# Performance work log

Hardware: AMD Instinct MI355X
Metric: run time of the kernel (lower is better)

The kernel has to match this reference:

```python
import jax, jax.numpy as jnp
import numpy as np

NODE_DIM = 64
OUT_DIM = 64
EDGE_DIM = 64
N_NODES = 50000
N_EDGES = 800000
BN_EPS = 1e-5


def _batchnorm(x, gamma, beta):
    # training-mode BatchNorm1d: biased batch statistics
    mean = jnp.mean(x, axis=0)
    var = jnp.mean((x - mean) ** 2, axis=0)
    return (x - mean) * jax.lax.rsqrt(var + BN_EPS) * gamma + beta


def setup_inputs() -> dict:
    key = jax.random.key(0)
    ks = jax.random.split(key, 16)
    s = 0.05  # weight init scale
    inp = {
        "em": jax.random.normal(ks[0], (N_NODES, NODE_DIM), jnp.float32),
        "edge_index": jax.random.randint(ks[1], (2, N_EDGES), 0, N_NODES, jnp.int64),
        "edge_features": jax.random.normal(ks[2], (N_EDGES, EDGE_DIM), jnp.float32),
        # GINEConv edge linear (edge_dim -> node_dim)
        "W_le": jax.random.normal(ks[3], (EDGE_DIM, NODE_DIM), jnp.float32) * s,
        "b_le": jnp.zeros((NODE_DIM,), jnp.float32),
        # GINEConv nn: Linear(node_dim, out) -> ReLU -> Linear(out, out)
        "W1": jax.random.normal(ks[4], (NODE_DIM, OUT_DIM), jnp.float32) * s,
        "b1": jnp.zeros((OUT_DIM,), jnp.float32),
        "W2": jax.random.normal(ks[5], (OUT_DIM, OUT_DIM), jnp.float32) * s,
        "b2": jnp.zeros((OUT_DIM,), jnp.float32),
        # x BatchNorm affine
        "gx": jnp.ones((OUT_DIM,), jnp.float32),
        "bx": jnp.zeros((OUT_DIM,), jnp.float32),
        # edge MLP: (edge_dim + 2*out) -> out -> out -> out
        "We1": jax.random.normal(ks[6], (EDGE_DIM + 2 * OUT_DIM, OUT_DIM), jnp.float32) * s,
        "be1": jnp.zeros((OUT_DIM,), jnp.float32),
        "We2": jax.random.normal(ks[7], (OUT_DIM, OUT_DIM), jnp.float32) * s,
        "be2": jnp.zeros((OUT_DIM,), jnp.float32),
        "We3": jax.random.normal(ks[8], (OUT_DIM, OUT_DIM), jnp.float32) * s,
        "be3": jnp.zeros((OUT_DIM,), jnp.float32),
        # edge BatchNorm affine
        "ge": jnp.ones((OUT_DIM,), jnp.float32),
        "be": jnp.zeros((OUT_DIM,), jnp.float32),
    }
    return inp


def reference(em, edge_index, edge_features, W_le, b_le, W1, b1, W2, b2, gx, bx,
              We1, be1, We2, be2, We3, be3, ge, be):
    src, dst = edge_index[0], edge_index[1]
    # GINEConv: msg = relu(x_j + lin(edge_attr)), sum-aggregated at target
    msg = jax.nn.relu(em[src] + edge_features @ W_le + b_le)  # [E, node_dim]
    aggr = jax.ops.segment_sum(msg, dst, num_segments=em.shape[0])  # [N, node_dim]
    h = em + aggr  # eps = 0
    h = jax.nn.relu(h @ W1 + b1) @ W2 + b2  # [N, out]
    x_em = jax.nn.relu(_batchnorm(h, gx, bx))
    # edge update: concat(x_em[src], x_em[dst], edge_features)
    edge_mess = jnp.concatenate([x_em[src], x_em[dst], edge_features], axis=1)
    e = jax.nn.relu(edge_mess @ We1 + be1)
    e = jax.nn.relu(e @ We2 + be2)
    e = e @ We3 + be3
    edge_out = jax.nn.relu(_batchnorm(e, ge, be))
    return x_em, edge_out
```

## Files before the change

### kernel.cpp

```cpp
#include <hip/hip_runtime.h>
#include <cstddef>

#define NN 50000
#define NE 800000

typedef __bf16 bf16x8 __attribute__((ext_vector_type(8)));
typedef float  f32x4  __attribute__((ext_vector_type(4)));

__device__ __forceinline__ bf16x8 ldfrag(const __bf16* __restrict__ wfr, int f, int lane) {
    return *reinterpret_cast<const bf16x8*>(wfr + (size_t)(f * 64 + lane) * 8);
}
__device__ __forceinline__ f32x4 mfma16(bf16x8 a, bf16x8 b, f32x4 c) {
    return __builtin_amdgcn_mfma_f32_16x16x32_bf16(a, b, c, 0, 0, 0);
}
__device__ __forceinline__ bool idx_is64(const int* eidx) {
    return ((eidx[1] | eidx[3] | eidx[5] | eidx[7]) == 0);
}
__device__ __forceinline__ int ld_src(const int* eidx, bool is64, int e) {
    return is64 ? eidx[(size_t)2 * e] : eidx[e];
}
__device__ __forceinline__ int ld_dst(const int* eidx, bool is64, int e) {
    return is64 ? eidx[2 * ((size_t)NE + e)] : eidx[(size_t)NE + e];
}

__global__ __launch_bounds__(256) void prep(const float* __restrict__ wle, const float* __restrict__ w1,
                                            const float* __restrict__ w2, const float* __restrict__ we1,
                                            const float* __restrict__ we2, const float* __restrict__ we3,
                                            __bf16* __restrict__ wfr) {
    int sid = blockIdx.x * 256 + threadIdx.x;
    int f = sid >> 6, lane = sid & 63;
    const float* W; int fo;
    if (f < 8)       { W = wle; fo = 0; }
    else if (f < 16) { W = w1;  fo = 8; }
    else if (f < 24) { W = w2;  fo = 16; }
    else if (f < 48) { W = we1; fo = 24; }
    else if (f < 56) { W = we2; fo = 48; }
    else             { W = we3; fo = 56; }
    int lf = f - fo, kt = lf >> 2, nt = lf & 3;
    int g = lane >> 4, c = lane & 15;
#pragma unroll
    for (int b = 0; b < 8; b++) {
        int k = kt * 32 + g * 8 + b;
        int n = nt * 16 + c;
        wfr[(size_t)(f * 64 + lane) * 8 + b] = (__bf16)W[(size_t)k * 64 + n];
    }
}

__global__ __launch_bounds__(256) void k1(const float* __restrict__ em, const int* __restrict__ eidx,
                                          const float* __restrict__ ef, const __bf16* __restrict__ wfr,
                                          const float* __restrict__ ble, float* __restrict__ nodebuf) {
    __shared__ __bf16 Ash[64][72];
    const int t = threadIdx.x;
    const int base = blockIdx.x * 64;
    {
        const int r = t >> 2, seg = t & 3;
        const float4* p = reinterpret_cast<const float4*>(ef + (size_t)(base + r) * 64 + seg * 16);
#pragma unroll
        for (int i = 0; i < 4; i++) {
            float4 v = p[i];
            int cb = seg * 16 + i * 4;
            Ash[r][cb + 0] = (__bf16)v.x; Ash[r][cb + 1] = (__bf16)v.y;
            Ash[r][cb + 2] = (__bf16)v.z; Ash[r][cb + 3] = (__bf16)v.w;
        }
    }
    const bool is64 = idx_is64(eidx);
    __syncthreads();
    const int lane = t & 63, w = t >> 6, c = lane & 15, g = lane >> 4;
    const int arow = w * 16 + c;
    f32x4 acc[4] = {{0.f,0.f,0.f,0.f},{0.f,0.f,0.f,0.f},{0.f,0.f,0.f,0.f},{0.f,0.f,0.f,0.f}};
#pragma unroll
    for (int kt = 0; kt < 2; kt++) {
        bf16x8 a = *reinterpret_cast<const bf16x8*>(&Ash[arow][kt * 32 + g * 8]);
#pragma unroll
        for (int nt = 0; nt < 4; nt++) acc[nt] = mfma16(a, ldfrag(wfr, kt * 4 + nt, lane), acc[nt]);
    }
#pragma unroll
    for (int rr = 0; rr < 4; rr++) {
        int e = base + w * 16 + g * 4 + rr;
        int sn = ld_src(eidx, is64, e);
        int dn = ld_dst(eidx, is64, e);
#pragma unroll
        for (int nt = 0; nt < 4; nt++) {
            int col = nt * 16 + c;
            float v = acc[nt][rr] + ble[col] + em[(size_t)sn * 64 + col];
            if (v > 0.f) atomicAdd(&nodebuf[(size_t)dn * 64 + col], v);
        }
    }
}

__global__ __launch_bounds__(256) void k2(const float* __restrict__ em, float* __restrict__ nb,
                                          const __bf16* __restrict__ wfr, const float* __restrict__ b1,
                                          const float* __restrict__ b2, float* __restrict__ sums) {
    __shared__ __bf16 Ash[64][72];
    __shared__ __bf16 Ysh[64][72];
    __shared__ float bs[128];
    const int t = threadIdx.x;
    const int base = blockIdx.x * 64;
    if (t < 128) bs[t] = 0.f;
    {
        const int r = t >> 2, seg = t & 3;
        const int row = base + r;
        if (row < NN) {
            const float4* pe = reinterpret_cast<const float4*>(em + (size_t)row * 64 + seg * 16);
            const float4* pa = reinterpret_cast<const float4*>(nb + (size_t)row * 64 + seg * 16);
#pragma unroll
            for (int i = 0; i < 4; i++) {
                float4 a = pe[i], b = pa[i];
                int cb = seg * 16 + i * 4;
                Ash[r][cb + 0] = (__bf16)(a.x + b.x); Ash[r][cb + 1] = (__bf16)(a.y + b.y);
                Ash[r][cb + 2] = (__bf16)(a.z + b.z); Ash[r][cb + 3] = (__bf16)(a.w + b.w);
            }
        } else {
#pragma unroll
            for (int j = 0; j < 16; j++) Ash[r][seg * 16 + j] = (__bf16)0.f;
        }
    }
    __syncthreads();
    const int lane = t & 63, w = t >> 6, c = lane & 15, g = lane >> 4;
    const int arow = w * 16 + c;
    f32x4 a1[4] = {{0.f,0.f,0.f,0.f},{0.f,0.f,0.f,0.f},{0.f,0.f,0.f,0.f},{0.f,0.f,0.f,0.f}};
#pragma unroll
    for (int kt = 0; kt < 2; kt++) {
        bf16x8 a = *reinterpret_cast<const bf16x8*>(&Ash[arow][kt * 32 + g * 8]);
#pragma unroll
        for (int nt = 0; nt < 4; nt++) a1[nt] = mfma16(a, ldfrag(wfr, 8 + kt * 4 + nt, lane), a1[nt]);
    }
#pragma unroll
    for (int nt = 0; nt < 4; nt++) {
        float bb = b1[nt * 16 + c];
#pragma unroll
        for (int rr = 0; rr < 4; rr++) {
            float v = a1[nt][rr] + bb;
            v = v > 0.f ? v : 0.f;
            Ysh[w * 16 + g * 4 + rr][nt * 16 + c] = (__bf16)v;
        }
    }
    __syncthreads();
    f32x4 a2[4] = {{0.f,0.f,0.f,0.f},{0.f,0.f,0.f,0.f},{0.f,0.f,0.f,0.f},{0.f,0.f,0.f,0.f}};
#pragma unroll
    for (int kt = 0; kt < 2; kt++) {
        bf16x8 a = *reinterpret_cast<const bf16x8*>(&Ysh[arow][kt * 32 + g * 8]);
#pragma unroll
        for (int nt = 0; nt < 4; nt++) a2[nt] = mfma16(a, ldfrag(wfr, 16 + kt * 4 + nt, lane), a2[nt]);
    }
#pragma unroll
    for (int nt = 0; nt < 4; nt++) {
        int col = nt * 16 + c;
        float bb = b2[col];
        float ss = 0.f, qq = 0.f;
#pragma unroll
        for (int rr = 0; rr < 4; rr++) {
            int row = base + w * 16 + g * 4 + rr;
            if (row < NN) {
                float v = a2[nt][rr] + bb;
                nb[(size_t)row * 64 + col] = v;
                ss += v; qq += v * v;
            }
        }
        ss += __shfl_xor(ss, 16); ss += __shfl_xor(ss, 32);
        qq += __shfl_xor(qq, 16); qq += __shfl_xor(qq, 32);
        if (g == 0) { atomicAdd(&bs[col], ss); atomicAdd(&bs[64 + col], qq); }
    }
    __syncthreads();
    if (t < 128) atomicAdd(&sums[t], bs[t]);
}

__global__ __launch_bounds__(256) void k3(float* __restrict__ nb, const float* __restrict__ sums,
                                          const float* __restrict__ gx, const float* __restrict__ bx,
                                          __bf16* __restrict__ wsx) {
    size_t i4 = (size_t)(blockIdx.x * 256 + threadIdx.x) * 4;
    int col0 = (int)(i4 & 63);
    float4 v = *reinterpret_cast<const float4*>(nb + i4);
    const float* pv = reinterpret_cast<const float*>(&v);
    float o[4]; short so[4];
#pragma unroll
    for (int j = 0; j < 4; j++) {
        int col = col0 + j;
        float m   = sums[col] * (1.0f / 50000.0f);
        float var = sums[64 + col] * (1.0f / 50000.0f) - m * m;
        float inv = rsqrtf(var + 1e-5f);
        float x = (pv[j] - m) * inv * gx[col] + bx[col];
        x = x > 0.f ? x : 0.f;
        o[j] = x;
        so[j] = __builtin_bit_cast(short, (__bf16)x);
    }
    *reinterpret_cast<float4*>(nb + i4) = make_float4(o[0], o[1], o[2], o[3]);
    *reinterpret_cast<short4*>(wsx + i4) = make_short4(so[0], so[1], so[2], so[3]);
}

__global__ __launch_bounds__(256) void k4(const int* __restrict__ eidx, const float* __restrict__ ef,
                                          const __bf16* __restrict__ wsx, const __bf16* __restrict__ wfr,
                                          const float* __restrict__ be1, const float* __restrict__ be2,
                                          const float* __restrict__ be3, float* __restrict__ eout,
                                          float* __restrict__ pws) {
    __shared__ __bf16 Ash[64][200];
    __shared__ __bf16 Ysh[64][72];
    __shared__ float bs[128];
    const int t = threadIdx.x;
    const int base = blockIdx.x * 64;
    if (t < 128) bs[t] = 0.f;
    const bool is64 = idx_is64(eidx);
    {
        const int r = t >> 2, seg = t & 3;
        const int e = base + r;
        const int sn = ld_src(eidx, is64, e);
        const int dn = ld_dst(eidx, is64, e);
        const uint4* ps = reinterpret_cast<const uint4*>(wsx + ((size_t)sn << 6)) + seg * 2;
        const uint4* pd = reinterpret_cast<const uint4*>(wsx + ((size_t)dn << 6)) + seg * 2;
        *reinterpret_cast<uint4*>(&Ash[r][seg * 16]) = ps[0];
        *reinterpret_cast<uint4*>(&Ash[r][seg * 16 + 8]) = ps[1];
        *reinterpret_cast<uint4*>(&Ash[r][64 + seg * 16]) = pd[0];
        *reinterpret_cast<uint4*>(&Ash[r][64 + seg * 16 + 8]) = pd[1];
        const float4* pf = reinterpret_cast<const float4*>(ef + (size_t)e * 64 + seg * 16);
#pragma unroll
        for (int i = 0; i < 4; i++) {
            float4 v = pf[i];
            int cb = 128 + seg * 16 + i * 4;
            Ash[r][cb + 0] = (__bf16)v.x; Ash[r][cb + 1] = (__bf16)v.y;
            Ash[r][cb + 2] = (__bf16)v.z; Ash[r][cb + 3] = (__bf16)v.w;
        }
    }
    __syncthreads();
    const int lane = t & 63, w = t >> 6, c = lane & 15, g = lane >> 4;
    const int arow = w * 16 + c;
    f32x4 a1[4] = {{0.f,0.f,0.f,0.f},{0.f,0.f,0.f,0.f},{0.f,0.f,0.f,0.f},{0.f,0.f,0.f,0.f}};
#pragma unroll
    for (int kt = 0; kt < 6; kt++) {
        bf16x8 a = *reinterpret_cast<const bf16x8*>(&Ash[arow][kt * 32 + g * 8]);
#pragma unroll
        for (int nt = 0; nt < 4; nt++) a1[nt] = mfma16(a, ldfrag(wfr, 24 + kt * 4 + nt, lane), a1[nt]);
    }
#pragma unroll
    for (int nt = 0; nt < 4; nt++) {
        float bb = be1[nt * 16 + c];
#pragma unroll
        for (int rr = 0; rr < 4; rr++) {
            float v = a1[nt][rr] + bb;
            v = v > 0.f ? v : 0.f;
            Ysh[w * 16 + g * 4 + rr][nt * 16 + c] = (__bf16)v;
        }
    }
    __syncthreads();
    f32x4 a2[4] = {{0.f,0.f,0.f,0.f},{0.f,0.f,0.f,0.f},{0.f,0.f,0.f,0.f},{0.f,0.f,0.f,0.f}};
#pragma unroll
    for (int kt = 0; kt < 2; kt++) {
        bf16x8 a = *reinterpret_cast<const bf16x8*>(&Ysh[arow][kt * 32 + g * 8]);
#pragma unroll
        for (int nt = 0; nt < 4; nt++) a2[nt] = mfma16(a, ldfrag(wfr, 48 + kt * 4 + nt, lane), a2[nt]);
    }
    __syncthreads();
#pragma unroll
    for (int nt = 0; nt < 4; nt++) {
        float bb = be2[nt * 16 + c];
#pragma unroll
        for (int rr = 0; rr < 4; rr++) {
            float v = a2[nt][rr] + bb;
            v = v > 0.f ? v : 0.f;
            Ysh[w * 16 + g * 4 + rr][nt * 16 + c] = (__bf16)v;
        }
    }
    __syncthreads();
    f32x4 a3[4] = {{0.f,0.f,0.f,0.f},{0.f,0.f,0.f,0.f},{0.f,0.f,0.f,0.f},{0.f,0.f,0.f,0.f}};
#pragma unroll
    for (int kt = 0; kt < 2; kt++) {
        bf16x8 a = *reinterpret_cast<const bf16x8*>(&Ysh[arow][kt * 32 + g * 8]);
#pragma unroll
        for (int nt = 0; nt < 4; nt++) a3[nt] = mfma16(a, ldfrag(wfr, 56 + kt * 4 + nt, lane), a3[nt]);
    }
#pragma unroll
    for (int nt = 0; nt < 4; nt++) {
        int col = nt * 16 + c;
        float bb = be3[col];
        float ss = 0.f, qq = 0.f;
#pragma unroll
        for (int rr = 0; rr < 4; rr++) {
            int e = base + w * 16 + g * 4 + rr;
            float v = a3[nt][rr] + bb;
            eout[(size_t)e * 64 + col] = v;
            ss += v; qq += v * v;
        }
        ss += __shfl_xor(ss, 16); ss += __shfl_xor(ss, 32);
        qq += __shfl_xor(qq, 16); qq += __shfl_xor(qq, 32);
        if (g == 0) { atomicAdd(&bs[col], ss); atomicAdd(&bs[64 + col], qq); }
    }
    __syncthreads();
    if (t < 128) pws[(size_t)t * 12500 + blockIdx.x] = bs[t];
}

__global__ __launch_bounds__(256) void k4r(const float* __restrict__ pws, float* __restrict__ sums) {
    int b = blockIdx.x;
    float s = 0.f;
    for (int i = threadIdx.x; i < 12500; i += 256) s += pws[(size_t)b * 12500 + i];
#pragma unroll
    for (int m = 32; m >= 1; m >>= 1) s += __shfl_xor(s, m);
    __shared__ float acc4[4];
    int lane = threadIdx.x & 63, wid = threadIdx.x >> 6;
    if (lane == 0) acc4[wid] = s;
    __syncthreads();
    if (threadIdx.x == 0) sums[128 + b] = acc4[0] + acc4[1] + acc4[2] + acc4[3];
}

__global__ __launch_bounds__(256) void k5(float* __restrict__ eo, const float* __restrict__ sums,
                                          const float* __restrict__ ge, const float* __restrict__ be) {
    size_t i4 = (size_t)(blockIdx.x * 256 + threadIdx.x) * 4;
    int col0 = (int)(i4 & 63);
    float4 v = *reinterpret_cast<const float4*>(eo + i4);
    const float* pv = reinterpret_cast<const float*>(&v);
    float o[4];
#pragma unroll
    for (int j = 0; j < 4; j++) {
        int col = col0 + j;
        float m   = sums[128 + col] * (1.0f / 800000.0f);
        float var = sums[192 + col] * (1.0f / 800000.0f) - m * m;
        float inv = rsqrtf(var + 1e-5f);
        float x = (pv[j] - m) * inv * ge[col] + be[col];
        o[j] = x > 0.f ? x : 0.f;
    }
    *reinterpret_cast<float4*>(eo + i4) = make_float4(o[0], o[1], o[2], o[3]);
}

extern "C" void kernel_launch(void* const* d_in, const int* in_sizes, int n_in,
                              void* d_out, int out_size, void* d_ws, size_t ws_size,
                              hipStream_t stream) {
    const float* em   = (const float*)d_in[0];
    const int*   eidx = (const int*)d_in[1];
    const float* ef   = (const float*)d_in[2];
    const float* W_le = (const float*)d_in[3];
    const float* b_le = (const float*)d_in[4];
    const float* W1   = (const float*)d_in[5];
    const float* b1   = (const float*)d_in[6];
    const float* W2   = (const float*)d_in[7];
    const float* b2   = (const float*)d_in[8];
    const float* gx   = (const float*)d_in[9];
    const float* bx   = (const float*)d_in[10];
    const float* We1  = (const float*)d_in[11];
    const float* be1  = (const float*)d_in[12];
    const float* We2  = (const float*)d_in[13];
    const float* be2  = (const float*)d_in[14];
    const float* We3  = (const float*)d_in[15];
    const float* be3  = (const float*)d_in[16];
    const float* ge   = (const float*)d_in[17];
    const float* be   = (const float*)d_in[18];

    float* out = (float*)d_out;
    float* nodebuf = out;
    float* eout = out + (size_t)NN * 64;

    float*  sums = (float*)d_ws;
    __bf16* wfr  = (__bf16*)((char*)d_ws + 1024);
    __bf16* wsx  = (__bf16*)((char*)d_ws + 1024 + 65536);
    float*  pws  = (float*)((char*)d_ws + 1024 + 65536 + (size_t)NN * 64 * 2);

    hipMemsetAsync(sums, 0, 256 * sizeof(float), stream);
    hipMemsetAsync(nodebuf, 0, (size_t)NN * 64 * sizeof(float), stream);

    prep<<<16, 256, 0, stream>>>(W_le, W1, W2, We1, We2, We3, wfr);
    k1<<<NE / 64, 256, 0, stream>>>(em, eidx, ef, wfr, b_le, nodebuf);
    k2<<<(NN + 63) / 64, 256, 0, stream>>>(em, nodebuf, wfr, b1, b2, sums);
    k3<<<(NN * 64) / 1024, 256, 0, stream>>>(nodebuf, sums, gx, bx, wsx);
    k4<<<NE / 64, 256, 0, stream>>>(eidx, ef, wsx, wfr, be1, be2, be3, eout, pws);
    k4r<<<128, 256, 0, stream>>>(pws, sums);
    k5<<<((size_t)NE * 64) / 1024, 256, 0, stream>>>(eout, sums, ge, be);
}
```

Baseline: 487.1 us.

## Load MFMA operands straight to registers and cache bf16 edge features

The k1, k2 and k4 kernels now load their A-operand fragments from global memory directly into registers in MFMA layout, instead of staging them through shared memory with block barriers. The intra-warp Ysh handoffs lose their __syncthreads, since each wave only reads rows it wrote itself. k1 also writes a bf16 copy of the edge features to workspace when space allows, so k4 reads half the bytes instead of reconverting fp32. The trade-offs are extra writes in k1 and less coalesced per-lane fragment loads, and the bf16 path depends on the workspace size.

Result: slower. 519.1 us, median of 4 (+6.6%).

```diff
diff --git a/kernel.cpp b/kernel.cpp
--- a/kernel.cpp
+++ b/kernel.cpp
@@ -21,6 +21,14 @@
 }
 __device__ __forceinline__ int ld_dst(const int* eidx, bool is64, int e) {
     return is64 ? eidx[2 * ((size_t)NE + e)] : eidx[(size_t)NE + e];
+}
+__device__ __forceinline__ bf16x8 cvt8(const float* __restrict__ p) {
+    float4 v0 = *reinterpret_cast<const float4*>(p);
+    float4 v1 = *reinterpret_cast<const float4*>(p + 4);
+    bf16x8 r;
+    r[0] = (__bf16)v0.x; r[1] = (__bf16)v0.y; r[2] = (__bf16)v0.z; r[3] = (__bf16)v0.w;
+    r[4] = (__bf16)v1.x; r[5] = (__bf16)v1.y; r[6] = (__bf16)v1.z; r[7] = (__bf16)v1.w;
+    return r;
 }
 
 __global__ __launch_bounds__(256) void prep(const float* __restrict__ wle, const float* __restrict__ w1,
@@ -48,32 +56,24 @@
 
 __global__ __launch_bounds__(256) void k1(const float* __restrict__ em, const int* __restrict__ eidx,
                                           const float* __restrict__ ef, const __bf16* __restrict__ wfr,
-                                          const float* __restrict__ ble, float* __restrict__ nodebuf) {
-    __shared__ __bf16 Ash[64][72];
+                                          const float* __restrict__ ble, float* __restrict__ nodebuf,
+                                          __bf16* __restrict__ ef16) {
     const int t = threadIdx.x;
     const int base = blockIdx.x * 64;
-    {
-        const int r = t >> 2, seg = t & 3;
-        const float4* p = reinterpret_cast<const float4*>(ef + (size_t)(base + r) * 64 + seg * 16);
-#pragma unroll
-        for (int i = 0; i < 4; i++) {
-            float4 v = p[i];
-            int cb = seg * 16 + i * 4;
-            Ash[r][cb + 0] = (__bf16)v.x; Ash[r][cb + 1] = (__bf16)v.y;
-            Ash[r][cb + 2] = (__bf16)v.z; Ash[r][cb + 3] = (__bf16)v.w;
-        }
-    }
+    const int lane = t & 63, w = t >> 6, c = lane & 15, g = lane >> 4;
+    const int erow = base + w * 16 + c;
     const bool is64 = idx_is64(eidx);
-    __syncthreads();
-    const int lane = t & 63, w = t >> 6, c = lane & 15, g = lane >> 4;
-    const int arow = w * 16 + c;
+    bf16x8 a[2];
+#pragma unroll
+    for (int kt = 0; kt < 2; kt++) {
+        a[kt] = cvt8(ef + (size_t)erow * 64 + kt * 32 + g * 8);
+        if (ef16) *reinterpret_cast<bf16x8*>(ef16 + (size_t)erow * 64 + kt * 32 + g * 8) = a[kt];
+    }
     f32x4 acc[4] = {{0.f,0.f,0.f,0.f},{0.f,0.f,0.f,0.f},{0.f,0.f,0.f,0.f},{0.f,0.f,0.f,0.f}};
 #pragma unroll
-    for (int kt = 0; kt < 2; kt++) {
-        bf16x8 a = *reinterpret_cast<const bf16x8*>(&Ash[arow][kt * 32 + g * 8]);
-#pragma unroll
-        for (int nt = 0; nt < 4; nt++) acc[nt] = mfma16(a, ldfrag(wfr, kt * 4 + nt, lane), acc[nt]);
-    }
+    for (int kt = 0; kt < 2; kt++)
+#pragma unroll
+        for (int nt = 0; nt < 4; nt++) acc[nt] = mfma16(a[kt], ldfrag(wfr, kt * 4 + nt, lane), acc[nt]);
 #pragma unroll
     for (int rr = 0; rr < 4; rr++) {
         int e = base + w * 16 + g * 4 + rr;
@@ -91,40 +91,35 @@
 __global__ __launch_bounds__(256) void k2(const float* __restrict__ em, float* __restrict__ nb,
                                           const __bf16* __restrict__ wfr, const float* __restrict__ b1,
                                           const float* __restrict__ b2, float* __restrict__ sums) {
-    __shared__ __bf16 Ash[64][72];
     __shared__ __bf16 Ysh[64][72];
     __shared__ float bs[128];
     const int t = threadIdx.x;
     const int base = blockIdx.x * 64;
     if (t < 128) bs[t] = 0.f;
-    {
-        const int r = t >> 2, seg = t & 3;
-        const int row = base + r;
-        if (row < NN) {
-            const float4* pe = reinterpret_cast<const float4*>(em + (size_t)row * 64 + seg * 16);
-            const float4* pa = reinterpret_cast<const float4*>(nb + (size_t)row * 64 + seg * 16);
-#pragma unroll
-            for (int i = 0; i < 4; i++) {
-                float4 a = pe[i], b = pa[i];
-                int cb = seg * 16 + i * 4;
-                Ash[r][cb + 0] = (__bf16)(a.x + b.x); Ash[r][cb + 1] = (__bf16)(a.y + b.y);
-                Ash[r][cb + 2] = (__bf16)(a.z + b.z); Ash[r][cb + 3] = (__bf16)(a.w + b.w);
-            }
-        } else {
-#pragma unroll
-            for (int j = 0; j < 16; j++) Ash[r][seg * 16 + j] = (__bf16)0.f;
-        }
-    }
     __syncthreads();
     const int lane = t & 63, w = t >> 6, c = lane & 15, g = lane >> 4;
-    const int arow = w * 16 + c;
+    const int arow = base + w * 16 + c;
+    const size_t rl = (size_t)(arow < NN ? arow : NN - 1) * 64;
+    bf16x8 a[2];
+#pragma unroll
+    for (int kt = 0; kt < 2; kt++) {
+        int off = kt * 32 + g * 8;
+        float4 e0 = *reinterpret_cast<const float4*>(em + rl + off);
+        float4 e1 = *reinterpret_cast<const float4*>(em + rl + off + 4);
+        float4 n0 = *reinterpret_cast<const float4*>(nb + rl + off);
+        float4 n1 = *reinterpret_cast<const float4*>(nb + rl + off + 4);
+        bf16x8 r;
+        r[0] = (__bf16)(e0.x + n0.x); r[1] = (__bf16)(e0.y + n0.y);
+        r[2] = (__bf16)(e0.z + n0.z); r[3] = (__bf16)(e0.w + n0.w);
+        r[4] = (__bf16)(e1.x + n1.x); r[5] = (__bf16)(e1.y + n1.y);
+        r[6] = (__bf16)(e1.z + n1.z); r[7] = (__bf16)(e1.w + n1.w);
+        a[kt] = r;
+    }
     f32x4 a1[4] = {{0.f,0.f,0.f,0.f},{0.f,0.f,0.f,0.f},{0.f,0.f,0.f,0.f},{0.f,0.f,0.f,0.f}};
 #pragma unroll
-    for (int kt = 0; kt < 2; kt++) {
-        bf16x8 a = *reinterpret_cast<const bf16x8*>(&Ash[arow][kt * 32 + g * 8]);
-#pragma unroll
-        for (int nt = 0; nt < 4; nt++) a1[nt] = mfma16(a, ldfrag(wfr, 8 + kt * 4 + nt, lane), a1[nt]);
-    }
+    for (int kt = 0; kt < 2; kt++)
+#pragma unroll
+        for (int nt = 0; nt < 4; nt++) a1[nt] = mfma16(a[kt], ldfrag(wfr, 8 + kt * 4 + nt, lane), a1[nt]);
 #pragma unroll
     for (int nt = 0; nt < 4; nt++) {
         float bb = b1[nt * 16 + c];
@@ -135,14 +130,15 @@
             Ysh[w * 16 + g * 4 + rr][nt * 16 + c] = (__bf16)v;
         }
     }
-    __syncthreads();
+    bf16x8 ya[2];
+#pragma unroll
+    for (int kt = 0; kt < 2; kt++)
+        ya[kt] = *reinterpret_cast<const bf16x8*>(&Ysh[w * 16 + c][kt * 32 + g * 8]);
     f32x4 a2[4] = {{0.f,0.f,0.f,0.f},{0.f,0.f,0.f,0.f},{0.f,0.f,0.f,0.f},{0.f,0.f,0.f,0.f}};
 #pragma unroll
-    for (int kt = 0; kt < 2; kt++) {
-        bf16x8 a = *reinterpret_cast<const bf16x8*>(&Ysh[arow][kt * 32 + g * 8]);
-#pragma unroll
-        for (int nt = 0; nt < 4; nt++) a2[nt] = mfma16(a, ldfrag(wfr, 16 + kt * 4 + nt, lane), a2[nt]);
-    }
+    for (int kt = 0; kt < 2; kt++)
+#pragma unroll
+        for (int nt = 0; nt < 4; nt++) a2[nt] = mfma16(ya[kt], ldfrag(wfr, 16 + kt * 4 + nt, lane), a2[nt]);
 #pragma unroll
     for (int nt = 0; nt < 4; nt++) {
         int col = nt * 16 + c;
@@ -189,47 +185,44 @@
 }
 
 __global__ __launch_bounds__(256) void k4(const int* __restrict__ eidx, const float* __restrict__ ef,
-                                          const __bf16* __restrict__ wsx, const __bf16* __restrict__ wfr,
+                                          const __bf16* __restrict__ ef16, const __bf16* __restrict__ wsx,
+                                          const __bf16* __restrict__ wfr,
                                           const float* __restrict__ be1, const float* __restrict__ be2,
                                           const float* __restrict__ be3, float* __restrict__ eout,
                                           float* __restrict__ pws) {
-    __shared__ __bf16 Ash[64][200];
     __shared__ __bf16 Ysh[64][72];
     __shared__ float bs[128];
     const int t = threadIdx.x;
     const int base = blockIdx.x * 64;
     if (t < 128) bs[t] = 0.f;
+    __syncthreads();
+    const int lane = t & 63, w = t >> 6, c = lane & 15, g = lane >> 4;
+    const int erow = base + w * 16 + c;
     const bool is64 = idx_is64(eidx);
-    {
-        const int r = t >> 2, seg = t & 3;
-        const int e = base + r;
-        const int sn = ld_src(eidx, is64, e);
-        const int dn = ld_dst(eidx, is64, e);
-        const uint4* ps = reinterpret_cast<const uint4*>(wsx + ((size_t)sn << 6)) + seg * 2;
-        const uint4* pd = reinterpret_cast<const uint4*>(wsx + ((size_t)dn << 6)) + seg * 2;
-        *reinterpret_cast<uint4*>(&Ash[r][seg * 16]) = ps[0];
-        *reinterpret_cast<uint4*>(&Ash[r][seg * 16 + 8]) = ps[1];
-        *reinterpret_cast<uint4*>(&Ash[r][64 + seg * 16]) = pd[0];
-        *reinterpret_cast<uint4*>(&Ash[r][64 + seg * 16 + 8]) = pd[1];
-        const float4* pf = reinterpret_cast<const float4*>(ef + (size_t)e * 64 + seg * 16);
-#pragma unroll
-        for (int i = 0; i < 4; i++) {
-            float4 v = pf[i];
-            int cb = 128 + seg * 16 + i * 4;
-            Ash[r][cb + 0] = (__bf16)v.x; Ash[r][cb + 1] = (__bf16)v.y;
-            Ash[r][cb + 2] = (__bf16)v.z; Ash[r][cb + 3] = (__bf16)v.w;
-        }
-    }
-    __syncthreads();
-    const int lane = t & 63, w = t >> 6, c = lane & 15, g = lane >> 4;
-    const int arow = w * 16 + c;
+    const int sn = ld_src(eidx, is64, erow);
+    const int dn = ld_dst(eidx, is64, erow);
+    bf16x8 xs[2], xd[2], ea[2];
+#pragma unroll
+    for (int kt = 0; kt < 2; kt++) {
+        int off = kt * 32 + g * 8;
+        xs[kt] = *reinterpret_cast<const bf16x8*>(wsx + (size_t)sn * 64 + off);
+        xd[kt] = *reinterpret_cast<const bf16x8*>(wsx + (size_t)dn * 64 + off);
+        ea[kt] = ef16 ? *reinterpret_cast<const bf16x8*>(ef16 + (size_t)erow * 64 + off)
+                      : cvt8(ef + (size_t)erow * 64 + off);
+    }
     f32x4 a1[4] = {{0.f,0.f,0.f,0.f},{0.f,0.f,0.f,0.f},{0.f,0.f,0.f,0.f},{0.f,0.f,0.f,0.f}};
 #pragma unroll
-    for (int kt = 0; kt < 6; kt++) {
-        bf16x8 a = *reinterpret_cast<const bf16x8*>(&Ash[arow][kt * 32 + g * 8]);
-#pragma unroll
-        for (int nt = 0; nt < 4; nt++) a1[nt] = mfma16(a, ldfrag(wfr, 24 + kt * 4 + nt, lane), a1[nt]);
-    }
+    for (int kt = 0; kt < 2; kt++)
+#pragma unroll
+        for (int nt = 0; nt < 4; nt++) a1[nt] = mfma16(xs[kt], ldfrag(wfr, 24 + kt * 4 + nt, lane), a1[nt]);
+#pragma unroll
+    for (int kt = 0; kt < 2; kt++)
+#pragma unroll
+        for (int nt = 0; nt < 4; nt++) a1[nt] = mfma16(xd[kt], ldfrag(wfr, 32 + kt * 4 + nt, lane), a1[nt]);
+#pragma unroll
+    for (int kt = 0; kt < 2; kt++)
+#pragma unroll
+        for (int nt = 0; nt < 4; nt++) a1[nt] = mfma16(ea[kt], ldfrag(wfr, 40 + kt * 4 + nt, lane), a1[nt]);
 #pragma unroll
     for (int nt = 0; nt < 4; nt++) {
         float bb = be1[nt * 16 + c];
@@ -240,15 +233,15 @@
             Ysh[w * 16 + g * 4 + rr][nt * 16 + c] = (__bf16)v;
         }
     }
-    __syncthreads();
+    bf16x8 ya[2];
+#pragma unroll
+    for (int kt = 0; kt < 2; kt++)
+        ya[kt] = *reinterpret_cast<const bf16x8*>(&Ysh[w * 16 + c][kt * 32 + g * 8]);
     f32x4 a2[4] = {{0.f,0.f,0.f,0.f},{0.f,0.f,0.f,0.f},{0.f,0.f,0.f,0.f},{0.f,0.f,0.f,0.f}};
 #pragma unroll
-    for (int kt = 0; kt < 2; kt++) {
-        bf16x8 a = *reinterpret_cast<const bf16x8*>(&Ysh[arow][kt * 32 + g * 8]);
-#pragma unroll
-        for (int nt = 0; nt < 4; nt++) a2[nt] = mfma16(a, ldfrag(wfr, 48 + kt * 4 + nt, lane), a2[nt]);
-    }
-    __syncthreads();
+    for (int kt = 0; kt < 2; kt++)
+#pragma unroll
+        for (int nt = 0; nt < 4; nt++) a2[nt] = mfma16(ya[kt], ldfrag(wfr, 48 + kt * 4 + nt, lane), a2[nt]);
 #pragma unroll
     for (int nt = 0; nt < 4; nt++) {
         float bb = be2[nt * 16 + c];
@@ -259,14 +252,14 @@
             Ysh[w * 16 + g * 4 + rr][nt * 16 + c] = (__bf16)v;
         }
     }
-    __syncthreads();
+#pragma unroll
+    for (int kt = 0; kt < 2; kt++)
+        ya[kt] = *reinterpret_cast<const bf16x8*>(&Ysh[w * 16 + c][kt * 32 + g * 8]);
     f32x4 a3[4] = {{0.f,0.f,0.f,0.f},{0.f,0.f,0.f,0.f},{0.f,0.f,0.f,0.f},{0.f,0.f,0.f,0.f}};
 #pragma unroll
-    for (int kt = 0; kt < 2; kt++) {
-        bf16x8 a = *reinterpret_cast<const bf16x8*>(&Ysh[arow][kt * 32 + g * 8]);
-#pragma unroll
-        for (int nt = 0; nt < 4; nt++) a3[nt] = mfma16(a, ldfrag(wfr, 56 + kt * 4 + nt, lane), a3[nt]);
-    }
+    for (int kt = 0; kt < 2; kt++)
+#pragma unroll
+        for (int nt = 0; nt < 4; nt++) a3[nt] = mfma16(ya[kt], ldfrag(wfr, 56 + kt * 4 + nt, lane), a3[nt]);
 #pragma unroll
     for (int nt = 0; nt < 4; nt++) {
         int col = nt * 16 + c;
@@ -325,19 +318,13 @@
     const float* em   = (const float*)d_in[0];
     const int*   eidx = (const int*)d_in[1];
     const float* ef   = (const float*)d_in[2];
-    const float* W_le = (const float*)d_in[3];
     const float* b_le = (const float*)d_in[4];
-    const float* W1   = (const float*)d_in[5];
     const float* b1   = (const float*)d_in[6];
-    const float* W2   = (const float*)d_in[7];
     const float* b2   = (const float*)d_in[8];
     const float* gx   = (const float*)d_in[9];
     const float* bx   = (const float*)d_in[10];
-    const float* We1  = (const float*)d_in[11];
     const float* be1  = (const float*)d_in[12];
-    const float* We2  = (const float*)d_in[13];
     const float* be2  = (const float*)d_in[14];
-    const float* We3  = (const float*)d_in[15];
     const float* be3  = (const float*)d_in[16];
     const float* ge   = (const float*)d_in[17];
     const float* be   = (const float*)d_in[18];
@@ -350,15 +337,19 @@
     __bf16* wfr  = (__bf16*)((char*)d_ws + 1024);
     __bf16* wsx  = (__bf16*)((char*)d_ws + 1024 + 65536);
     float*  pws  = (float*)((char*)d_ws + 1024 + 65536 + (size_t)NN * 64 * 2);
+    size_t  base_need = 1024 + 65536 + (size_t)NN * 64 * 2 + (size_t)128 * 12500 * 4;
+    __bf16* ef16 = (ws_size >= base_need + (size_t)NE * 64 * 2)
+                   ? (__bf16*)((char*)d_ws + base_need) : nullptr;
 
     hipMemsetAsync(sums, 0, 256 * sizeof(float), stream);
     hipMemsetAsync(nodebuf, 0, (size_t)NN * 64 * sizeof(float), stream);
 
-    prep<<<16, 256, 0, stream>>>(W_le, W1, W2, We1, We2, We3, wfr);
-    k1<<<NE / 64, 256, 0, stream>>>(em, eidx, ef, wfr, b_le, nodebuf);
+    prep<<<16, 256, 0, stream>>>((const float*)d_in[3], (const float*)d_in[5], (const float*)d_in[7],
+                                 (const float*)d_in[11], (const float*)d_in[13], (const float*)d_in[15], wfr);
+    k1<<<NE / 64, 256, 0, stream>>>(em, eidx, ef, wfr, b_le, nodebuf, ef16);
     k2<<<(NN + 63) / 64, 256, 0, stream>>>(em, nodebuf, wfr, b1, b2, sums);
     k3<<<(NN * 64) / 1024, 256, 0, stream>>>(nodebuf, sums, gx, bx, wsx);
-    k4<<<NE / 64, 256, 0, stream>>>(eidx, ef, wsx, wfr, be1, be2, be3, eout, pws);
+    k4<<<NE / 64, 256, 0, stream>>>(eidx, ef, ef16, wsx, wfr, be1, be2, be3, eout, pws);
     k4r<<<128, 256, 0, stream>>>(pws, sums);
     k5<<<((size_t)NE * 64) / 1024, 256, 0, stream>>>(eout, sums, ge, be);
 }
```
